# Kernel optimization log

Measured on AMD Instinct MI355X. Metric: run time of the kernel, lower is better.

The kernel has to match this reference:

```python
import jax, jax.numpy as jnp
import numpy as np
from jax import lax

B, S, D, T = 128, 512, 512, 64
OUT = 3


def setup_inputs() -> dict:
    key = jax.random.key(0)
    ks = jax.random.split(key, 16)
    sd = 0.05
    return {
        "e_all": jax.random.normal(ks[0], (B, S, D), jnp.float32),
        "e_last": jax.random.normal(ks[1], (1, B, D), jnp.float32),
        "target": jax.random.normal(ks[2], (B, T, OUT), jnp.float32),
        # attention params
        "Wa": jax.random.normal(ks[3], (D, D), jnp.float32) * sd,
        "ba": jnp.zeros((D,), jnp.float32),
        "Ua": jax.random.normal(ks[4], (D, D), jnp.float32) * sd,
        "bu": jnp.zeros((D,), jnp.float32),
        "Va_w": jax.random.normal(ks[5], (1, D), jnp.float32) * sd,
        "Va_b": jnp.zeros((1,), jnp.float32),
        # GRU params (PyTorch layout: [3D, in], gates order r,z,n)
        "W_ih": jax.random.normal(ks[6], (3 * D, D + OUT), jnp.float32) * sd,
        "b_ih": jnp.zeros((3 * D,), jnp.float32),
        "W_hh": jax.random.normal(ks[7], (3 * D, D), jnp.float32) * sd,
        "b_hh": jnp.zeros((3 * D,), jnp.float32),
        # output projection
        "W_out": jax.random.normal(ks[8], (OUT, D), jnp.float32) * sd,
        "b_out": jnp.zeros((OUT,), jnp.float32),
    }


def reference(e_all, e_last, target, Wa, ba, Ua, bu, Va_w, Va_b,
              W_ih, b_ih, W_hh, b_hh, W_out, b_out):
    # Precompute Ua(keys): keys are fixed across timesteps (same math as per-step).
    Uk = jnp.einsum('bsd,ed->bse', e_all, Ua) + bu        # [B,S,D]
    va = Va_w[0]                                          # [D]

    def step(h, x):
        # h: [B,D] decoder hidden; x: [B,3] decoder input (dropout is eval/identity)
        q = h @ Wa.T + ba                                  # [B,D]
        scores = jnp.einsum('bsd,d->bs', jnp.tanh(q[:, None, :] + Uk), va) + Va_b[0]
        w = jax.nn.softmax(scores, axis=-1)                # [B,S]
        ctx = jnp.einsum('bs,bsd->bd', w, e_all)           # [B,D]
        gin = jnp.concatenate([ctx, x], axis=-1)           # [B,D+3]  (attn first)
        gi = gin @ W_ih.T + b_ih                           # [B,3D]
        gh = h @ W_hh.T + b_hh                             # [B,3D]
        i_r, i_z, i_n = jnp.split(gi, 3, axis=-1)
        h_r, h_z, h_n = jnp.split(gh, 3, axis=-1)
        r = jax.nn.sigmoid(i_r + h_r)
        z = jax.nn.sigmoid(i_z + h_z)
        n = jnp.tanh(i_n + r * h_n)
        h_new = (1.0 - z) * n + z * h                      # [B,D]
        out = h_new @ W_out.T + b_out                      # [B,3]
        return h_new, (out, w)

    # teacher forcing: step 0 sees zeros, step i sees target[:, i-1]
    xs = jnp.concatenate([jnp.zeros((1, B, OUT), e_all.dtype),
                          jnp.swapaxes(target[:, :T - 1, :], 0, 1)], axis=0)  # [T,B,3]
    hT, (outs, attns) = lax.scan(step, e_last[0], xs)
    d_outputs = jnp.swapaxes(outs, 0, 1)     # [B,T,3]
    cross_attn = jnp.swapaxes(attns, 0, 1)   # [B,T,S]
    return d_outputs, hT[None], cross_attn
```

## Files before the change

### kernel.cpp

```cpp
#include <hip/hip_runtime.h>
#include <cstdint>

constexpr int BB = 128;
constexpr int SS = 512;
constexpr int DD = 512;
constexpr int TT = 64;
constexpr int OO = 3;

constexpr float C2LE = 2.8853900817779268f;

typedef __attribute__((ext_vector_type(8))) short bf16x8;
typedef __attribute__((ext_vector_type(4))) float f32x4;
typedef unsigned int u32x4 __attribute__((ext_vector_type(4)));

__device__ __forceinline__ float tanh_fast(float x) {
  float e = __expf(2.0f * x);
  return 1.0f - 2.0f / (e + 1.0f);
}
__device__ __forceinline__ float sigmoid_fast(float x) {
  return 1.0f / (1.0f + __expf(-x));
}
__device__ __forceinline__ unsigned short f2bf(float f) {
  uint32_t u = __float_as_uint(f);
  uint32_t r = (u + 0x7FFFu + ((u >> 16) & 1u)) >> 16;
  return (unsigned short)r;
}
__device__ __forceinline__ float bf2f(unsigned short h) {
  return __uint_as_float((uint32_t)h << 16);
}
__device__ __forceinline__ float2 bfx2(uint32_t u) {
  float2 r;
  r.x = __uint_as_float(u << 16);
  r.y = __uint_as_float(u & 0xFFFF0000u);
  return r;
}
__device__ __forceinline__ float fexp2(float x) {
#if __has_builtin(__builtin_amdgcn_exp2f)
  return __builtin_amdgcn_exp2f(x);
#else
  return exp2f(x);
#endif
}
__device__ __forceinline__ float frcp(float x) {
#if __has_builtin(__builtin_amdgcn_rcpf)
  return __builtin_amdgcn_rcpf(x);
#else
  return 1.0f / x;
#endif
}

__device__ __forceinline__ void gstore(float* p, float v) {
  __hip_atomic_store(p, v, __ATOMIC_RELAXED, __HIP_MEMORY_SCOPE_AGENT);
}
__device__ __forceinline__ float gload(const float* p) {
  return __hip_atomic_load(p, __ATOMIC_RELAXED, __HIP_MEMORY_SCOPE_AGENT);
}

__device__ __forceinline__ void pair_barrier(unsigned int* cnt,
                                             unsigned int target) {
  asm volatile("s_waitcnt vmcnt(0)" ::: "memory");
  __syncthreads();
  if (threadIdx.x == 0) {
    __hip_atomic_fetch_add(cnt, 1u, __ATOMIC_RELAXED, __HIP_MEMORY_SCOPE_AGENT);
    while (__hip_atomic_load(cnt, __ATOMIC_RELAXED,
                             __HIP_MEMORY_SCOPE_AGENT) < target)
      __builtin_amdgcn_s_sleep(2);
  }
  __syncthreads();
}

__global__ __launch_bounds__(256) void gemm_uk_mfma(
    const unsigned short* __restrict__ A, const unsigned short* __restrict__ Bw,
    const float* __restrict__ bias, unsigned short* __restrict__ Uk) {
  __shared__ unsigned short Asb[128 * 40];
  __shared__ unsigned short Bsb[128 * 40];
  const int tid = threadIdx.x;
  const int m0 = blockIdx.y * 128, n0 = blockIdx.x * 128;
  const int w = tid >> 6, l = tid & 63;
  const int wr = w >> 1, wc = w & 1;
  const int lm = l & 15, kg = l >> 4;

  f32x4 acc[4][4] = {};

  for (int kc = 0; kc < 512; kc += 32) {
    uint4 av[2], bv[2];
#pragma unroll
    for (int p = 0; p < 2; ++p) {
      int u = tid + p * 256;
      int r = u >> 2, ko = (u & 3) * 8;
      av[p] = *(const uint4*)(A + (size_t)(m0 + r) * 512 + kc + ko);
      bv[p] = *(const uint4*)(Bw + (size_t)(n0 + r) * 512 + kc + ko);
    }
    __syncthreads();
#pragma unroll
    for (int p = 0; p < 2; ++p) {
      int u = tid + p * 256;
      int r = u >> 2, ko = (u & 3) * 8;
      *(uint4*)&Asb[r * 40 + ko] = av[p];
      *(uint4*)&Bsb[r * 40 + ko] = bv[p];
    }
    __syncthreads();
    bf16x8 af[4], bfr[4];
#pragma unroll
    for (int i = 0; i < 4; ++i) {
      af[i]  = *(const bf16x8*)&Asb[(wr * 64 + i * 16 + lm) * 40 + kg * 8];
      bfr[i] = *(const bf16x8*)&Bsb[(wc * 64 + i * 16 + lm) * 40 + kg * 8];
    }
#pragma unroll
    for (int i = 0; i < 4; ++i)
#pragma unroll
      for (int j = 0; j < 4; ++j)
        acc[i][j] = __builtin_amdgcn_mfma_f32_16x16x32_bf16(af[i], bfr[j],
                                                            acc[i][j], 0, 0, 0);
  }

  const int row_base = m0 + wr * 64;
  const int col_base = n0 + wc * 64;
#pragma unroll
  for (int j = 0; j < 4; ++j) {
    const int col = col_base + j * 16 + lm;
    const float bu = bias[col];
#pragma unroll
    for (int i = 0; i < 4; ++i) {
      const int r0 = row_base + i * 16 + kg * 4;
#pragma unroll
      for (int rr = 0; rr < 4; ++rr)
        Uk[(size_t)(r0 + rr) * 512 + col] = f2bf(C2LE * (acc[i][j][rr] + bu));
    }
  }
}

__global__ __launch_bounds__(256) void conv_bf(const float* __restrict__ in,
                                               unsigned short* __restrict__ outp) {
  size_t idx = ((size_t)blockIdx.x * 256 + threadIdx.x) * 8;
  const float4* p = (const float4*)(in + idx);
  float4 a = p[0], b = p[1];
  uint4 r;
  r.x = f2bf(a.x) | ((uint32_t)f2bf(a.y) << 16);
  r.y = f2bf(a.z) | ((uint32_t)f2bf(a.w) << 16);
  r.z = f2bf(b.x) | ((uint32_t)f2bf(b.y) << 16);
  r.w = f2bf(b.z) | ((uint32_t)f2bf(b.w) << 16);
  *(uint4*)(outp + idx) = r;
}

__global__ void prep_wq2t(const float* __restrict__ Wa,
                          unsigned short* __restrict__ Wq2t) {
  int idx = blockIdx.x * 256 + threadIdx.x;
  int k = idx >> 9, j = idx & 511;
  Wq2t[idx] = f2bf(C2LE * Wa[(size_t)j * DD + k]);
}

__global__ void prep_wihT(const float* __restrict__ W_ih,
                          unsigned short* __restrict__ WihT) {
  int idx = blockIdx.x * 256 + threadIdx.x;
  int k = idx / 1536, col = idx % 1536;
  WihT[idx] = f2bf(W_ih[(size_t)col * (DD + OO) + k]);
}

__global__ void prep_whhT(const float* __restrict__ Whh,
                          unsigned short* __restrict__ WhhT) {
  int idx = blockIdx.x * 256 + threadIdx.x;
  int k = idx / 1536, col = idx % 1536;
  WhhT[idx] = f2bf(Whh[(size_t)col * DD + k]);
}

__global__ void prep_bq(const float* __restrict__ ba, float* __restrict__ bq) {
  int j = blockIdx.x * 256 + threadIdx.x;
  bq[j] = C2LE * ba[j];
}

__global__ __launch_bounds__(1024, 1) void decode_pairs(
    const unsigned short* __restrict__ Uk2, const unsigned short* __restrict__ e_bf,
    const unsigned short* __restrict__ Wq2t, const unsigned short* __restrict__ WihT,
    const unsigned short* __restrict__ WhhT, const float* __restrict__ bq,
    const float* __restrict__ W_ih, const float* __restrict__ b_ih,
    const float* __restrict__ b_hh, const float* __restrict__ e_last,
    const float* __restrict__ target, const float* __restrict__ Va_w,
    const float* __restrict__ W_out, const float* __restrict__ b_out,
    float* __restrict__ ctxp, char* __restrict__ bars,
    float* __restrict__ out_d, float* __restrict__ out_hT,
    float* __restrict__ out_attn) {
  const int blk = blockIdx.x, tid = threadIdx.x;
  const int b = blk >> 1, half = blk & 1;
  char* bar_base = bars + (size_t)b * 256;
  unsigned int* cnt = (unsigned int*)bar_base;
  float* stat4 = (float*)(bar_base + 16);
  unsigned int bc = 0;

  __shared__ float va_s[528];
  __shared__ float qv_s[528];
  __shared__ float h_s[512];
  __shared__ float pd_s[512];
  __shared__ float u_s[256];
  __shared__ float w_s[256];
  __shared__ float red_s[16];
  __shared__ float part[16 * 520];
  __shared__ float ctx_s[512];
  __shared__ float gis[768];
  __shared__ float ghs[768];

  float wxr0 = 0.f, wxr1 = 0.f, wxr2 = 0.f, bihr = 0.f, bhhr = 0.f;
  if (tid < 768) {
    const int gate = tid >> 8, dl = tid & 255;
    const int row = gate * 512 + half * 256 + dl;
    const float* wp = W_ih + (size_t)row * (DD + OO) + DD;
    wxr0 = wp[0]; wxr1 = wp[1]; wxr2 = wp[2];
    bihr = b_ih[row]; bhhr = b_hh[row];
  }
  if (tid < 512) va_s[(tid >> 7) * 132 + (tid & 127)] = Va_w[tid];
  __syncthreads();

  for (int t = 0; t < TT; ++t) {
    if (tid < 512) {
      h_s[tid] = (t == 0) ? e_last[(size_t)b * 512 + tid]
                          : gload(out_hT + (size_t)b * 512 + tid);
    }
    __syncthreads();
    {
      const int col = tid & 511, kb = tid >> 9;
      const unsigned short* wp = Wq2t + (size_t)(kb * 256) * 512 + col;
      const float* hb = &h_s[kb * 256];
      float acc = 0.f;
      for (int k0 = 0; k0 < 256; k0 += 8) {
        float4 hv0 = *(const float4*)&hb[k0];
        float4 hv1 = *(const float4*)&hb[k0 + 4];
        acc += hv0.x * bf2f(wp[(size_t)(k0 + 0) * 512]);
        acc += hv0.y * bf2f(wp[(size_t)(k0 + 1) * 512]);
        acc += hv0.z * bf2f(wp[(size_t)(k0 + 2) * 512]);
        acc += hv0.w * bf2f(wp[(size_t)(k0 + 3) * 512]);
        acc += hv1.x * bf2f(wp[(size_t)(k0 + 4) * 512]);
        acc += hv1.y * bf2f(wp[(size_t)(k0 + 5) * 512]);
        acc += hv1.z * bf2f(wp[(size_t)(k0 + 6) * 512]);
        acc += hv1.w * bf2f(wp[(size_t)(k0 + 7) * 512]);
      }
      if (kb) pd_s[col] = acc;
      __syncthreads();
      if (!kb) {
        float q = acc + pd_s[col] + bq[col];
        qv_s[(col >> 7) * 132 + (col & 127)] = q;
      }
      if (half == 0 && t > 0 && tid >= 512 && tid < 704) {
        const int o = (tid - 512) >> 6, ln = tid & 63;
        const float* wrow = W_out + (size_t)o * DD;
        float a = 0.f;
        for (int i = ln; i < DD; i += 64) a += h_s[i] * wrow[i];
#pragma unroll
        for (int off = 32; off; off >>= 1) a += __shfl_xor(a, off);
        if (ln == 0)
          out_d[((size_t)b * TT + (t - 1)) * OO + o] = a + b_out[o];
      }
    }
    __syncthreads();
    {
      const int sl = tid >> 2, qp = tid & 3;
      const u32x4* up = (const u32x4*)(Uk2 +
          ((size_t)b * SS + half * 256 + sl) * DD + qp * 128);
      const float* qb = &qv_s[qp * 132];
      const float* vb = &va_s[qp * 132];
      float acc = 0.f;
#pragma unroll 4
      for (int j = 0; j < 16; ++j) {
        u32x4 u = __builtin_nontemporal_load(up + j);
        float4 q0 = *(const float4*)&qb[j * 8], q1 = *(const float4*)&qb[j * 8 + 4];
        float4 v0 = *(const float4*)&vb[j * 8], v1 = *(const float4*)&vb[j * 8 + 4];
        float2 e0 = bfx2(u[0]), e1 = bfx2(u[1]), e2 = bfx2(u[2]), e3 = bfx2(u[3]);
        acc += v0.x * frcp(1.f + fexp2(q0.x + e0.x));
        acc += v0.y * frcp(1.f + fexp2(q0.y + e0.y));
        acc += v0.z * frcp(1.f + fexp2(q0.z + e1.x));
        acc += v0.w * frcp(1.f + fexp2(q0.w + e1.y));
        acc += v1.x * frcp(1.f + fexp2(q1.x + e2.x));
        acc += v1.y * frcp(1.f + fexp2(q1.y + e2.y));
        acc += v1.z * frcp(1.f + fexp2(q1.z + e3.x));
        acc += v1.w * frcp(1.f + fexp2(q1.w + e3.y));
      }
      acc += __shfl_xor(acc, 1);
      acc += __shfl_xor(acc, 2);
      if (qp == 0) u_s[sl] = -2.f * acc;
    }
    __syncthreads();
    {
      const int w4 = tid >> 6;
      float y = (tid < 256) ? u_s[tid] : -3.0e38f;
      float m = y;
#pragma unroll
      for (int off = 32; off; off >>= 1) m = fmaxf(m, __shfl_xor(m, off));
      if (w4 < 4 && (tid & 63) == 0) red_s[w4] = m;
      __syncthreads();
      const float gm =
          fmaxf(fmaxf(red_s[0], red_s[1]), fmaxf(red_s[2], red_s[3]));
      float e = (tid < 256) ? __expf(y - gm) : 0.f;
      float sm = e;
#pragma unroll
      for (int off = 32; off; off >>= 1) sm += __shfl_xor(sm, off);
      if (w4 < 4 && (tid & 63) == 0) red_s[8 + w4] = sm;
      __syncthreads();
      if (tid < 256) u_s[tid] = e;
      if (tid == 0) {
        gstore(&stat4[half * 2], gm);
        gstore(&stat4[half * 2 + 1],
               red_s[8] + red_s[9] + red_s[10] + red_s[11]);
      }
    }
    pair_barrier(cnt, 2 * (++bc));

    if (tid == 0) {
      red_s[8] = gload(&stat4[0]);
      red_s[9] = gload(&stat4[1]);
      red_s[10] = gload(&stat4[2]);
      red_s[11] = gload(&stat4[3]);
    }
    __syncthreads();
    {
      const float m0 = red_s[8], l0 = red_s[9], m1 = red_s[10], l1 = red_s[11];
      const float M = fmaxf(m0, m1);
      const float invZ = frcp(l0 * __expf(m0 - M) + l1 * __expf(m1 - M));
      const float al = __expf((half ? m1 : m0) - M) * invZ;
      if (tid < 256) {
        float wv = u_s[tid] * al;
        w_s[tid] = wv;
        __builtin_nontemporal_store(
            wv, out_attn + ((size_t)b * TT + t) * SS + half * 256 + tid);
      }
    }
    __syncthreads();
    {
      const int dsl = tid & 63, sg = tid >> 6;
      const unsigned short* eb =
          e_bf + ((size_t)b * SS + half * 256 + sg * 16) * DD + dsl * 8;
      float a0 = 0.f, a1 = 0.f, a2 = 0.f, a3 = 0.f;
      float a4 = 0.f, a5 = 0.f, a6 = 0.f, a7 = 0.f;
#pragma unroll 4
      for (int si = 0; si < 16; ++si) {
        u32x4 u = __builtin_nontemporal_load((const u32x4*)(eb + (size_t)si * DD));
        float ws = w_s[sg * 16 + si];
        float2 p0 = bfx2(u[0]), p1 = bfx2(u[1]), p2 = bfx2(u[2]), p3 = bfx2(u[3]);
        a0 += ws * p0.x; a1 += ws * p0.y;
        a2 += ws * p1.x; a3 += ws * p1.y;
        a4 += ws * p2.x; a5 += ws * p2.y;
        a6 += ws * p3.x; a7 += ws * p3.y;
      }
      float* pr = &part[sg * 520 + dsl * 8];
      float4 lo = {a0, a1, a2, a3}, hi = {a4, a5, a6, a7};
      *(float4*)&pr[0] = lo;
      *(float4*)&pr[4] = hi;
    }
    __syncthreads();
    if (tid < 512) {
      float r = 0.f;
#pragma unroll
      for (int sg = 0; sg < 16; ++sg) r += part[sg * 520 + tid];
      gstore(&ctxp[((size_t)b * 2 + half) * 512 + tid], r);
    }
    pair_barrier(cnt, 2 * (++bc));

    if (tid < 512)
      ctx_s[tid] = gload(&ctxp[(size_t)b * 2 * 512 + tid]) +
                   gload(&ctxp[((size_t)b * 2 + 1) * 512 + tid]);
    __syncthreads();
    if (tid < 768) {
      const int gate = tid >> 8, dl = tid & 255;
      const int col = gate * 512 + half * 256 + dl;
      const unsigned short* wi = WihT + col;
      const unsigned short* wh = WhhT + col;
      float ai = 0.f, ah = 0.f;
      for (int k0 = 0; k0 < 512; k0 += 8) {
        float4 c0 = *(const float4*)&ctx_s[k0];
        float4 c1 = *(const float4*)&ctx_s[k0 + 4];
        float4 h0 = *(const float4*)&h_s[k0];
        float4 h1 = *(const float4*)&h_s[k0 + 4];
        ai += c0.x * bf2f(wi[(size_t)(k0 + 0) * 1536]);
        ah += h0.x * bf2f(wh[(size_t)(k0 + 0) * 1536]);
        ai += c0.y * bf2f(wi[(size_t)(k0 + 1) * 1536]);
        ah += h0.y * bf2f(wh[(size_t)(k0 + 1) * 1536]);
        ai += c0.z * bf2f(wi[(size_t)(k0 + 2) * 1536]);
        ah += h0.z * bf2f(wh[(size_t)(k0 + 2) * 1536]);
        ai += c0.w * bf2f(wi[(size_t)(k0 + 3) * 1536]);
        ah += h0.w * bf2f(wh[(size_t)(k0 + 3) * 1536]);
        ai += c1.x * bf2f(wi[(size_t)(k0 + 4) * 1536]);
        ah += h1.x * bf2f(wh[(size_t)(k0 + 4) * 1536]);
        ai += c1.y * bf2f(wi[(size_t)(k0 + 5) * 1536]);
        ah += h1.y * bf2f(wh[(size_t)(k0 + 5) * 1536]);
        ai += c1.z * bf2f(wi[(size_t)(k0 + 6) * 1536]);
        ah += h1.z * bf2f(wh[(size_t)(k0 + 6) * 1536]);
        ai += c1.w * bf2f(wi[(size_t)(k0 + 7) * 1536]);
        ah += h1.w * bf2f(wh[(size_t)(k0 + 7) * 1536]);
      }
      float x0 = 0.f, x1 = 0.f, x2 = 0.f;
      if (t > 0) {
        const float* xp = target + ((size_t)b * TT + (t - 1)) * OO;
        x0 = xp[0]; x1 = xp[1]; x2 = xp[2];
      }
      gis[tid] = ai + bihr + x0 * wxr0 + x1 * wxr1 + x2 * wxr2;
      ghs[tid] = ah + bhhr;
    }
    __syncthreads();
    if (tid < 256) {
      const int d = half * 256 + tid;
      float r_ = sigmoid_fast(gis[tid] + ghs[tid]);
      float z_ = sigmoid_fast(gis[256 + tid] + ghs[256 + tid]);
      float n_ = tanh_fast(gis[512 + tid] + r_ * ghs[512 + tid]);
      float hnew = (1.f - z_) * n_ + z_ * h_s[d];
      gstore(out_hT + (size_t)b * 512 + d, hnew);
    }
    pair_barrier(cnt, 2 * (++bc));
  }

  if (half == 0) {
    if (tid < 512) h_s[tid] = gload(out_hT + (size_t)b * 512 + tid);
    __syncthreads();
    if (tid < 192) {
      const int o = tid >> 6, ln = tid & 63;
      const float* wrow = W_out + (size_t)o * DD;
      float a = 0.f;
      for (int i = ln; i < DD; i += 64) a += h_s[i] * wrow[i];
#pragma unroll
      for (int off = 32; off; off >>= 1) a += __shfl_xor(a, off);
      if (ln == 0)
        out_d[((size_t)b * TT + (TT - 1)) * OO + o] = a + b_out[o];
    }
  }
}

extern "C" void kernel_launch(void* const* d_in, const int* in_sizes, int n_in,
                              void* d_out, int out_size, void* d_ws, size_t ws_size,
                              hipStream_t stream) {
  const float* e_all  = (const float*)d_in[0];
  const float* e_last = (const float*)d_in[1];
  const float* target = (const float*)d_in[2];
  const float* Wa     = (const float*)d_in[3];
  const float* ba     = (const float*)d_in[4];
  const float* Ua     = (const float*)d_in[5];
  const float* bu     = (const float*)d_in[6];
  const float* Va_w   = (const float*)d_in[7];
  const float* W_ih   = (const float*)d_in[9];
  const float* b_ih   = (const float*)d_in[10];
  const float* W_hh   = (const float*)d_in[11];
  const float* b_hh   = (const float*)d_in[12];
  const float* W_out  = (const float*)d_in[13];
  const float* b_out  = (const float*)d_in[14];

  float* out      = (float*)d_out;
  float* out_d    = out;
  float* out_hT   = out + (size_t)BB * TT * OO;
  float* out_attn = out_hT + (size_t)BB * DD;

  char* wsB = (char*)d_ws;
  unsigned short* Uk2   = (unsigned short*)wsB;
  unsigned short* e_bfp = (unsigned short*)(wsB + 67108864);
  unsigned short* Wq2t  = (unsigned short*)(wsB + 134217728);
  unsigned short* WihT  = (unsigned short*)(wsB + 134742016);
  unsigned short* WhhT  = (unsigned short*)(wsB + 136314880);
  float* bq             = (float*)(wsB + 137887744);
  float* ctxp           = (float*)(wsB + 137889792);
  char* bars            = wsB + 138414080;
  unsigned short* Ua_bf = (unsigned short*)(wsB + 137889792);

  prep_wq2t<<<(DD * DD) / 256, 256, 0, stream>>>(Wa, Wq2t);
  prep_wihT<<<(512 * 1536) / 256, 256, 0, stream>>>(W_ih, WihT);
  prep_whhT<<<(512 * 1536) / 256, 256, 0, stream>>>(W_hh, WhhT);
  prep_bq<<<2, 256, 0, stream>>>(ba, bq);
  conv_bf<<<(BB * SS * DD) / (8 * 256), 256, 0, stream>>>(e_all, e_bfp);
  conv_bf<<<(DD * DD) / (8 * 256), 256, 0, stream>>>(Ua, Ua_bf);
  gemm_uk_mfma<<<dim3(DD / 128, (BB * SS) / 128), 256, 0, stream>>>(
      e_bfp, Ua_bf, bu, Uk2);

  hipMemsetAsync(bars, 0, 128 * 256, stream);

  decode_pairs<<<2 * BB, 1024, 0, stream>>>(
      Uk2, e_bfp, Wq2t, WihT, WhhT, bq, W_ih, b_ih, b_hh, e_last, target,
      Va_w, W_out, b_out, ctxp, bars, out_d, out_hT, out_attn);
}
```

Before: 5.523 ms.

## Split decode across quads of blocks by hidden dim, two batches per group

Reorganizes the persistent decoder so each group of four blocks handles two batch rows, with each block owning a 128-wide slice of the hidden dimension rather than half the sequence. Uk is stored in a transposed [b][dq][d][s] layout so each block streams only its own slice, and every weight read in the GRU and query GEMVs is reused across two batch rows. The output projection is folded into the step as per-slice partial sums. In exchange, each step now needs three cross-block barriers over four blocks, with score and context partials exchanged through global memory, and the per-element Uk and e loads are narrower scalar bf16 loads.

```diff
diff --git a/kernel.cpp b/kernel.cpp
--- a/kernel.cpp
+++ b/kernel.cpp
@@ -11,7 +11,6 @@
 
 typedef __attribute__((ext_vector_type(8))) short bf16x8;
 typedef __attribute__((ext_vector_type(4))) float f32x4;
-typedef unsigned int u32x4 __attribute__((ext_vector_type(4)));
 
 __device__ __forceinline__ float tanh_fast(float x) {
   float e = __expf(2.0f * x);
@@ -27,12 +26,6 @@
 }
 __device__ __forceinline__ float bf2f(unsigned short h) {
   return __uint_as_float((uint32_t)h << 16);
-}
-__device__ __forceinline__ float2 bfx2(uint32_t u) {
-  float2 r;
-  r.x = __uint_as_float(u << 16);
-  r.y = __uint_as_float(u & 0xFFFF0000u);
-  return r;
 }
 __device__ __forceinline__ float fexp2(float x) {
 #if __has_builtin(__builtin_amdgcn_exp2f)
@@ -56,8 +49,8 @@
   return __hip_atomic_load(p, __ATOMIC_RELAXED, __HIP_MEMORY_SCOPE_AGENT);
 }
 
-__device__ __forceinline__ void pair_barrier(unsigned int* cnt,
-                                             unsigned int target) {
+__device__ __forceinline__ void grp_barrier(unsigned int* cnt,
+                                            unsigned int target) {
   asm volatile("s_waitcnt vmcnt(0)" ::: "memory");
   __syncthreads();
   if (threadIdx.x == 0) {
@@ -71,7 +64,7 @@
 
 __global__ __launch_bounds__(256) void gemm_uk_mfma(
     const unsigned short* __restrict__ A, const unsigned short* __restrict__ Bw,
-    const float* __restrict__ bias, unsigned short* __restrict__ Uk) {
+    const float* __restrict__ bias, unsigned short* __restrict__ Ukq) {
   __shared__ unsigned short Asb[128 * 40];
   __shared__ unsigned short Bsb[128 * 40];
   const int tid = threadIdx.x;
@@ -119,13 +112,18 @@
 #pragma unroll
   for (int j = 0; j < 4; ++j) {
     const int col = col_base + j * 16 + lm;
-    const float bu = bias[col];
+    const int dqi = col >> 7, dpi = col & 127;
+    const float buv = bias[col];
 #pragma unroll
     for (int i = 0; i < 4; ++i) {
       const int r0 = row_base + i * 16 + kg * 4;
-#pragma unroll
-      for (int rr = 0; rr < 4; ++rr)
-        Uk[(size_t)(r0 + rr) * 512 + col] = f2bf(C2LE * (acc[i][j][rr] + bu));
+      const int bb = r0 >> 9, ss = r0 & 511;
+      ushort4 pk;
+      pk.x = f2bf(C2LE * (acc[i][j][0] + buv));
+      pk.y = f2bf(C2LE * (acc[i][j][1] + buv));
+      pk.z = f2bf(C2LE * (acc[i][j][2] + buv));
+      pk.w = f2bf(C2LE * (acc[i][j][3] + buv));
+      *(ushort4*)&Ukq[(((size_t)bb * 4 + dqi) * 128 + dpi) * 512 + ss] = pk;
     }
   }
 }
@@ -169,255 +167,215 @@
   bq[j] = C2LE * ba[j];
 }
 
-__global__ __launch_bounds__(1024, 1) void decode_pairs(
-    const unsigned short* __restrict__ Uk2, const unsigned short* __restrict__ e_bf,
+__global__ __launch_bounds__(1024, 1) void decode_quads(
+    const unsigned short* __restrict__ Ukq, const unsigned short* __restrict__ e_bf,
     const unsigned short* __restrict__ Wq2t, const unsigned short* __restrict__ WihT,
     const unsigned short* __restrict__ WhhT, const float* __restrict__ bq,
     const float* __restrict__ W_ih, const float* __restrict__ b_ih,
     const float* __restrict__ b_hh, const float* __restrict__ e_last,
     const float* __restrict__ target, const float* __restrict__ Va_w,
     const float* __restrict__ W_out, const float* __restrict__ b_out,
-    float* __restrict__ ctxp, char* __restrict__ bars,
+    float* __restrict__ scoresP, float* __restrict__ ctxg,
+    float* __restrict__ op, char* __restrict__ bars,
     float* __restrict__ out_d, float* __restrict__ out_hT,
     float* __restrict__ out_attn) {
   const int blk = blockIdx.x, tid = threadIdx.x;
-  const int b = blk >> 1, half = blk & 1;
-  char* bar_base = bars + (size_t)b * 256;
-  unsigned int* cnt = (unsigned int*)bar_base;
-  float* stat4 = (float*)(bar_base + 16);
+  const int g = blk >> 2, dq = blk & 3;
+  const int b0 = g * 2;
+  unsigned int* cnt = (unsigned int*)(bars + (size_t)g * 256);
   unsigned int bc = 0;
 
-  __shared__ float va_s[528];
-  __shared__ float qv_s[528];
-  __shared__ float h_s[512];
-  __shared__ float pd_s[512];
-  __shared__ float u_s[256];
-  __shared__ float w_s[256];
-  __shared__ float red_s[16];
-  __shared__ float part[16 * 520];
-  __shared__ float ctx_s[512];
-  __shared__ float gis[768];
-  __shared__ float ghs[768];
-
-  float wxr0 = 0.f, wxr1 = 0.f, wxr2 = 0.f, bihr = 0.f, bhhr = 0.f;
-  if (tid < 768) {
-    const int gate = tid >> 8, dl = tid & 255;
-    const int row = gate * 512 + half * 256 + dl;
+  __shared__ float h_s[2][512];
+  __shared__ float q2_sl[2][128];
+  __shared__ float pdq[3][2][128];
+  __shared__ float va_sl[128];
+  __shared__ float w_s[2][512];
+  __shared__ float red_s[2][16];
+  __shared__ float ctp[3][2][128];
+  __shared__ float c_s[2][512];
+  __shared__ f32x4 pd4[384];
+  __shared__ float gi_s[2][384];
+  __shared__ float gh_s[2][384];
+  __shared__ float hn_s[2][128];
+  __shared__ float x_s[2][3];
+
+  if (tid < 128) va_sl[tid] = Va_w[dq * 128 + tid];
+  float wx0 = 0.f, wx1 = 0.f, wx2 = 0.f, bi_r = 0.f, bh_r = 0.f;
+  if (tid < 384) {
+    const int cc = tid & 127, gate = (tid >> 7) % 3;
+    const int row = gate * 512 + dq * 128 + cc;
     const float* wp = W_ih + (size_t)row * (DD + OO) + DD;
-    wxr0 = wp[0]; wxr1 = wp[1]; wxr2 = wp[2];
-    bihr = b_ih[row]; bhhr = b_hh[row];
-  }
-  if (tid < 512) va_s[(tid >> 7) * 132 + (tid & 127)] = Va_w[tid];
+    wx0 = wp[0]; wx1 = wp[1]; wx2 = wp[2];
+    bi_r = b_ih[row]; bh_r = b_hh[row];
+  }
   __syncthreads();
 
   for (int t = 0; t < TT; ++t) {
-    if (tid < 512) {
-      h_s[tid] = (t == 0) ? e_last[(size_t)b * 512 + tid]
-                          : gload(out_hT + (size_t)b * 512 + tid);
-    }
-    __syncthreads();
-    {
-      const int col = tid & 511, kb = tid >> 9;
-      const unsigned short* wp = Wq2t + (size_t)(kb * 256) * 512 + col;
-      const float* hb = &h_s[kb * 256];
+    {
+      const int bl = tid >> 9, d = tid & 511;
+      h_s[bl][d] = (t == 0) ? e_last[(size_t)(b0 + bl) * 512 + d]
+                            : gload(out_hT + (size_t)(b0 + bl) * 512 + d);
+    }
+    if (dq == 0 && t > 0 && tid >= 1018) {
+      const int u = tid - 1018, bl = u / 3, o = u % 3;
+      float s = 0.f;
+#pragma unroll
+      for (int q = 0; q < 4; ++q)
+        s += gload(&op[(((size_t)(b0 + bl)) * 4 + q) * 3 + o]);
+      out_d[((size_t)(b0 + bl) * TT + (t - 1)) * OO + o] = s + b_out[o];
+    }
+    __syncthreads();
+    {
+      const int col = tid & 127, bl = (tid >> 7) & 1, kb = tid >> 8;
+      const int colg = dq * 128 + col;
       float acc = 0.f;
-      for (int k0 = 0; k0 < 256; k0 += 8) {
-        float4 hv0 = *(const float4*)&hb[k0];
-        float4 hv1 = *(const float4*)&hb[k0 + 4];
-        acc += hv0.x * bf2f(wp[(size_t)(k0 + 0) * 512]);
-        acc += hv0.y * bf2f(wp[(size_t)(k0 + 1) * 512]);
-        acc += hv0.z * bf2f(wp[(size_t)(k0 + 2) * 512]);
-        acc += hv0.w * bf2f(wp[(size_t)(k0 + 3) * 512]);
-        acc += hv1.x * bf2f(wp[(size_t)(k0 + 4) * 512]);
-        acc += hv1.y * bf2f(wp[(size_t)(k0 + 5) * 512]);
-        acc += hv1.z * bf2f(wp[(size_t)(k0 + 6) * 512]);
-        acc += hv1.w * bf2f(wp[(size_t)(k0 + 7) * 512]);
+#pragma unroll 8
+      for (int k = kb * 128; k < kb * 128 + 128; ++k)
+        acc += h_s[bl][k] * bf2f(Wq2t[(size_t)k * 512 + colg]);
+      if (kb) pdq[kb - 1][bl][col] = acc;
+      __syncthreads();
+      if (kb == 0)
+        q2_sl[bl][col] = acc + pdq[0][bl][col] + pdq[1][bl][col] +
+                         pdq[2][bl][col] + bq[colg];
+    }
+    __syncthreads();
+    {
+      const int bl = tid >> 9, s = tid & 511;
+      const unsigned short* up =
+          Ukq + (((size_t)(b0 + bl) * 4 + dq) * 128) * 512 + s;
+      float acc = 0.f;
+#pragma unroll 8
+      for (int dpi = 0; dpi < 128; ++dpi) {
+        unsigned short uv = __builtin_nontemporal_load(up + (size_t)dpi * 512);
+        acc += va_sl[dpi] * frcp(1.f + fexp2(q2_sl[bl][dpi] + bf2f(uv)));
       }
-      if (kb) pd_s[col] = acc;
+      gstore(&scoresP[(((size_t)(b0 + bl)) * 4 + dq) * 512 + s], acc);
+    }
+    grp_barrier(cnt, 4 * (++bc));
+
+    {
+      const int bl = tid >> 9, s = tid & 511;
+      const float* sp = &scoresP[((size_t)(b0 + bl)) * 4 * 512 + s];
+      float y = -2.f * (gload(sp) + gload(sp + 512) + gload(sp + 1024) +
+                        gload(sp + 1536));
+      float m = y;
+#pragma unroll
+      for (int off = 32; off; off >>= 1) m = fmaxf(m, __shfl_xor(m, off));
+      const int wv = (tid >> 6) & 7;
+      if ((tid & 63) == 0) red_s[bl][wv] = m;
       __syncthreads();
-      if (!kb) {
-        float q = acc + pd_s[col] + bq[col];
-        qv_s[(col >> 7) * 132 + (col & 127)] = q;
+      float gm = red_s[bl][0];
+#pragma unroll
+      for (int i = 1; i < 8; ++i) gm = fmaxf(gm, red_s[bl][i]);
+      float e = __expf(y - gm);
+      float sm = e;
+#pragma unroll
+      for (int off = 32; off; off >>= 1) sm += __shfl_xor(sm, off);
+      if ((tid & 63) == 0) red_s[bl][8 + wv] = sm;
+      __syncthreads();
+      float Z = red_s[bl][8];
+#pragma unroll
+      for (int i = 1; i < 8; ++i) Z += red_s[bl][8 + i];
+      float wgt = e * frcp(Z);
+      w_s[bl][s] = wgt;
+      if (s >= dq * 128 && s < dq * 128 + 128)
+        __builtin_nontemporal_store(
+            wgt, out_attn + ((size_t)(b0 + bl) * TT + t) * SS + s);
+    }
+    __syncthreads();
+    {
+      const int ch = tid >> 8, bl = (tid >> 7) & 1, dpi = tid & 127;
+      const unsigned short* eb =
+          e_bf + ((size_t)(b0 + bl) * 512 + ch * 128) * 512 + dq * 128 + dpi;
+      float acc = 0.f;
+#pragma unroll 8
+      for (int si = 0; si < 128; ++si) {
+        unsigned short uv = __builtin_nontemporal_load(eb + (size_t)si * 512);
+        acc += w_s[bl][ch * 128 + si] * bf2f(uv);
       }
-      if (half == 0 && t > 0 && tid >= 512 && tid < 704) {
-        const int o = (tid - 512) >> 6, ln = tid & 63;
-        const float* wrow = W_out + (size_t)o * DD;
-        float a = 0.f;
-        for (int i = ln; i < DD; i += 64) a += h_s[i] * wrow[i];
-#pragma unroll
-        for (int off = 32; off; off >>= 1) a += __shfl_xor(a, off);
-        if (ln == 0)
-          out_d[((size_t)b * TT + (t - 1)) * OO + o] = a + b_out[o];
+      if (ch) ctp[ch - 1][bl][dpi] = acc;
+      __syncthreads();
+      if (ch == 0)
+        gstore(&ctxg[(size_t)(b0 + bl) * 512 + dq * 128 + dpi],
+               acc + ctp[0][bl][dpi] + ctp[1][bl][dpi] + ctp[2][bl][dpi]);
+    }
+    grp_barrier(cnt, 4 * (++bc));
+
+    {
+      const int bl = tid >> 9, d = tid & 511;
+      c_s[bl][d] = gload(&ctxg[(size_t)(b0 + bl) * 512 + d]);
+    }
+    if (tid >= 1016 && tid < 1022) {
+      const int u = tid - 1016, bl = u / 3, o = u % 3;
+      x_s[bl][o] =
+          (t > 0) ? target[((size_t)(b0 + bl) * TT + (t - 1)) * OO + o] : 0.f;
+    }
+    __syncthreads();
+    {
+      float ai0 = 0.f, ai1 = 0.f, ah0 = 0.f, ah1 = 0.f;
+      int cc = 0, gate = 0;
+      if (tid < 768) {
+        cc = tid & 127; gate = (tid >> 7) % 3;
+        const int kb = tid / 384;
+        const int colg = gate * 512 + dq * 128 + cc;
+        const unsigned short* wi = WihT + colg;
+        const unsigned short* wh = WhhT + colg;
+#pragma unroll 8
+        for (int k = kb * 256; k < kb * 256 + 256; ++k) {
+          float wiv = bf2f(wi[(size_t)k * 1536]);
+          float whv = bf2f(wh[(size_t)k * 1536]);
+          ai0 += c_s[0][k] * wiv; ai1 += c_s[1][k] * wiv;
+          ah0 += h_s[0][k] * whv; ah1 += h_s[1][k] * whv;
+        }
+        if (tid >= 384) {
+          f32x4 v = {ai0, ai1, ah0, ah1};
+          pd4[gate * 128 + cc] = v;
+        }
       }
-    }
-    __syncthreads();
-    {
-      const int sl = tid >> 2, qp = tid & 3;
-      const u32x4* up = (const u32x4*)(Uk2 +
-          ((size_t)b * SS + half * 256 + sl) * DD + qp * 128);
-      const float* qb = &qv_s[qp * 132];
-      const float* vb = &va_s[qp * 132];
-      float acc = 0.f;
-#pragma unroll 4
-      for (int j = 0; j < 16; ++j) {
-        u32x4 u = __builtin_nontemporal_load(up + j);
-        float4 q0 = *(const float4*)&qb[j * 8], q1 = *(const float4*)&qb[j * 8 + 4];
-        float4 v0 = *(const float4*)&vb[j * 8], v1 = *(const float4*)&vb[j * 8 + 4];
-        float2 e0 = bfx2(u[0]), e1 = bfx2(u[1]), e2 = bfx2(u[2]), e3 = bfx2(u[3]);
-        acc += v0.x * frcp(1.f + fexp2(q0.x + e0.x));
-        acc += v0.y * frcp(1.f + fexp2(q0.y + e0.y));
-        acc += v0.z * frcp(1.f + fexp2(q0.z + e1.x));
-        acc += v0.w * frcp(1.f + fexp2(q0.w + e1.y));
-        acc += v1.x * frcp(1.f + fexp2(q1.x + e2.x));
-        acc += v1.y * frcp(1.f + fexp2(q1.y + e2.y));
-        acc += v1.z * frcp(1.f + fexp2(q1.z + e3.x));
-        acc += v1.w * frcp(1.f + fexp2(q1.w + e3.y));
+      __syncthreads();
+      if (tid < 384) {
+        f32x4 p = pd4[gate * 128 + cc];
+        const int gc = gate * 128 + cc;
+        gi_s[0][gc] = ai0 + p[0] + bi_r + x_s[0][0] * wx0 + x_s[0][1] * wx1 +
+                      x_s[0][2] * wx2;
+        gi_s[1][gc] = ai1 + p[1] + bi_r + x_s[1][0] * wx0 + x_s[1][1] * wx1 +
+                      x_s[1][2] * wx2;
+        gh_s[0][gc] = ah0 + p[2] + bh_r;
+        gh_s[1][gc] = ah1 + p[3] + bh_r;
       }
-      acc += __shfl_xor(acc, 1);
-      acc += __shfl_xor(acc, 2);
-      if (qp == 0) u_s[sl] = -2.f * acc;
-    }
-    __syncthreads();
-    {
-      const int w4 = tid >> 6;
-      float y = (tid < 256) ? u_s[tid] : -3.0e38f;
-      float m = y;
-#pragma unroll
-      for (int off = 32; off; off >>= 1) m = fmaxf(m, __shfl_xor(m, off));
-      if (w4 < 4 && (tid & 63) == 0) red_s[w4] = m;
-      __syncthreads();
-      const float gm =
-          fmaxf(fmaxf(red_s[0], red_s[1]), fmaxf(red_s[2], red_s[3]));
-      float e = (tid < 256) ? __expf(y - gm) : 0.f;
-      float sm = e;
-#pragma unroll
-      for (int off = 32; off; off >>= 1) sm += __shfl_xor(sm, off);
-      if (w4 < 4 && (tid & 63) == 0) red_s[8 + w4] = sm;
-      __syncthreads();
-      if (tid < 256) u_s[tid] = e;
-      if (tid == 0) {
-        gstore(&stat4[half * 2], gm);
-        gstore(&stat4[half * 2 + 1],
-               red_s[8] + red_s[9] + red_s[10] + red_s[11]);
-      }
-    }
-    pair_barrier(cnt, 2 * (++bc));
-
-    if (tid == 0) {
-      red_s[8] = gload(&stat4[0]);
-      red_s[9] = gload(&stat4[1]);
-      red_s[10] = gload(&stat4[2]);
-      red_s[11] = gload(&stat4[3]);
-    }
-    __syncthreads();
-    {
-      const float m0 = red_s[8], l0 = red_s[9], m1 = red_s[10], l1 = red_s[11];
-      const float M = fmaxf(m0, m1);
-      const float invZ = frcp(l0 * __expf(m0 - M) + l1 * __expf(m1 - M));
-      const float al = __expf((half ? m1 : m0) - M) * invZ;
-      if (tid < 256) {
-        float wv = u_s[tid] * al;
-        w_s[tid] = wv;
-        __builtin_nontemporal_store(
-            wv, out_attn + ((size_t)b * TT + t) * SS + half * 256 + tid);
-      }
-    }
-    __syncthreads();
-    {
-      const int dsl = tid & 63, sg = tid >> 6;
-      const unsigned short* eb =
-          e_bf + ((size_t)b * SS + half * 256 + sg * 16) * DD + dsl * 8;
-      float a0 = 0.f, a1 = 0.f, a2 = 0.f, a3 = 0.f;
-      float a4 = 0.f, a5 = 0.f, a6 = 0.f, a7 = 0.f;
-#pragma unroll 4
-      for (int si = 0; si < 16; ++si) {
-        u32x4 u = __builtin_nontemporal_load((const u32x4*)(eb + (size_t)si * DD));
-        float ws = w_s[sg * 16 + si];
-        float2 p0 = bfx2(u[0]), p1 = bfx2(u[1]), p2 = bfx2(u[2]), p3 = bfx2(u[3]);
-        a0 += ws * p0.x; a1 += ws * p0.y;
-        a2 += ws * p1.x; a3 += ws * p1.y;
-        a4 += ws * p2.x; a5 += ws * p2.y;
-        a6 += ws * p3.x; a7 += ws * p3.y;
-      }
-      float* pr = &part[sg * 520 + dsl * 8];
-      float4 lo = {a0, a1, a2, a3}, hi = {a4, a5, a6, a7};
-      *(float4*)&pr[0] = lo;
-      *(float4*)&pr[4] = hi;
-    }
-    __syncthreads();
-    if (tid < 512) {
-      float r = 0.f;
-#pragma unroll
-      for (int sg = 0; sg < 16; ++sg) r += part[sg * 520 + tid];
-      gstore(&ctxp[((size_t)b * 2 + half) * 512 + tid], r);
-    }
-    pair_barrier(cnt, 2 * (++bc));
-
-    if (tid < 512)
-      ctx_s[tid] = gload(&ctxp[(size_t)b * 2 * 512 + tid]) +
-                   gload(&ctxp[((size_t)b * 2 + 1) * 512 + tid]);
-    __syncthreads();
-    if (tid < 768) {
-      const int gate = tid >> 8, dl = tid & 255;
-      const int col = gate * 512 + half * 256 + dl;
-      const unsigned short* wi = WihT + col;
-      const unsigned short* wh = WhhT + col;
-      float ai = 0.f, ah = 0.f;
-      for (int k0 = 0; k0 < 512; k0 += 8) {
-        float4 c0 = *(const float4*)&ctx_s[k0];
-        float4 c1 = *(const float4*)&ctx_s[k0 + 4];
-        float4 h0 = *(const float4*)&h_s[k0];
-        float4 h1 = *(const float4*)&h_s[k0 + 4];
-        ai += c0.x * bf2f(wi[(size_t)(k0 + 0) * 1536]);
-        ah += h0.x * bf2f(wh[(size_t)(k0 + 0) * 1536]);
-        ai += c0.y * bf2f(wi[(size_t)(k0 + 1) * 1536]);
-        ah += h0.y * bf2f(wh[(size_t)(k0 + 1) * 1536]);
-        ai += c0.z * bf2f(wi[(size_t)(k0 + 2) * 1536]);
-        ah += h0.z * bf2f(wh[(size_t)(k0 + 2) * 1536]);
-        ai += c0.w * bf2f(wi[(size_t)(k0 + 3) * 1536]);
-        ah += h0.w * bf2f(wh[(size_t)(k0 + 3) * 1536]);
-        ai += c1.x * bf2f(wi[(size_t)(k0 + 4) * 1536]);
-        ah += h1.x * bf2f(wh[(size_t)(k0 + 4) * 1536]);
-        ai += c1.y * bf2f(wi[(size_t)(k0 + 5) * 1536]);
-        ah += h1.y * bf2f(wh[(size_t)(k0 + 5) * 1536]);
-        ai += c1.z * bf2f(wi[(size_t)(k0 + 6) * 1536]);
-        ah += h1.z * bf2f(wh[(size_t)(k0 + 6) * 1536]);
-        ai += c1.w * bf2f(wi[(size_t)(k0 + 7) * 1536]);
-        ah += h1.w * bf2f(wh[(size_t)(k0 + 7) * 1536]);
-      }
-      float x0 = 0.f, x1 = 0.f, x2 = 0.f;
-      if (t > 0) {
-        const float* xp = target + ((size_t)b * TT + (t - 1)) * OO;
-        x0 = xp[0]; x1 = xp[1]; x2 = xp[2];
-      }
-      gis[tid] = ai + bihr + x0 * wxr0 + x1 * wxr1 + x2 * wxr2;
-      ghs[tid] = ah + bhhr;
     }
     __syncthreads();
     if (tid < 256) {
-      const int d = half * 256 + tid;
-      float r_ = sigmoid_fast(gis[tid] + ghs[tid]);
-      float z_ = sigmoid_fast(gis[256 + tid] + ghs[256 + tid]);
-      float n_ = tanh_fast(gis[512 + tid] + r_ * ghs[512 + tid]);
-      float hnew = (1.f - z_) * n_ + z_ * h_s[d];
-      gstore(out_hT + (size_t)b * 512 + d, hnew);
-    }
-    pair_barrier(cnt, 2 * (++bc));
-  }
-
-  if (half == 0) {
-    if (tid < 512) h_s[tid] = gload(out_hT + (size_t)b * 512 + tid);
-    __syncthreads();
-    if (tid < 192) {
-      const int o = tid >> 6, ln = tid & 63;
-      const float* wrow = W_out + (size_t)o * DD;
-      float a = 0.f;
-      for (int i = ln; i < DD; i += 64) a += h_s[i] * wrow[i];
-#pragma unroll
-      for (int off = 32; off; off >>= 1) a += __shfl_xor(a, off);
+      const int bl = tid >> 7, cc = tid & 127;
+      const int d = dq * 128 + cc;
+      float r_ = sigmoid_fast(gi_s[bl][cc] + gh_s[bl][cc]);
+      float z_ = sigmoid_fast(gi_s[bl][128 + cc] + gh_s[bl][128 + cc]);
+      float n_ = tanh_fast(gi_s[bl][256 + cc] + r_ * gh_s[bl][256 + cc]);
+      float hnew = (1.f - z_) * n_ + z_ * h_s[bl][d];
+      gstore(out_hT + (size_t)(b0 + bl) * 512 + d, hnew);
+      hn_s[bl][cc] = hnew;
+    }
+    __syncthreads();
+    if (tid >= 256 && tid < 640) {
+      const int u = tid - 256, grp = u >> 6, ln = u & 63;
+      const int o = grp % 3, bl = grp / 3;
+      const float* wrow = W_out + (size_t)o * DD + dq * 128;
+      float acc = hn_s[bl][ln] * wrow[ln] + hn_s[bl][ln + 64] * wrow[ln + 64];
+#pragma unroll
+      for (int off = 32; off; off >>= 1) acc += __shfl_xor(acc, off);
       if (ln == 0)
-        out_d[((size_t)b * TT + (TT - 1)) * OO + o] = a + b_out[o];
-    }
+        gstore(&op[(((size_t)(b0 + bl)) * 4 + dq) * 3 + o], acc);
+    }
+    grp_barrier(cnt, 4 * (++bc));
+  }
+
+  if (dq == 0 && tid >= 1018) {
+    const int u = tid - 1018, bl = u / 3, o = u % 3;
+    float s = 0.f;
+#pragma unroll
+    for (int q = 0; q < 4; ++q)
+      s += gload(&op[(((size_t)(b0 + bl)) * 4 + q) * 3 + o]);
+    out_d[((size_t)(b0 + bl) * TT + (TT - 1)) * OO + o] = s + b_out[o];
   }
 }
 
@@ -445,14 +403,16 @@
   float* out_attn = out_hT + (size_t)BB * DD;
 
   char* wsB = (char*)d_ws;
-  unsigned short* Uk2   = (unsigned short*)wsB;
+  unsigned short* Ukq   = (unsigned short*)wsB;
   unsigned short* e_bfp = (unsigned short*)(wsB + 67108864);
   unsigned short* Wq2t  = (unsigned short*)(wsB + 134217728);
   unsigned short* WihT  = (unsigned short*)(wsB + 134742016);
   unsigned short* WhhT  = (unsigned short*)(wsB + 136314880);
   float* bq             = (float*)(wsB + 137887744);
-  float* ctxp           = (float*)(wsB + 137889792);
-  char* bars            = wsB + 138414080;
+  float* scoresP        = (float*)(wsB + 137889792);
+  float* ctxg           = (float*)(wsB + 138938368);
+  float* op             = (float*)(wsB + 139200512);
+  char* bars            = wsB + 139206656;
   unsigned short* Ua_bf = (unsigned short*)(wsB + 137889792);
 
   prep_wq2t<<<(DD * DD) / 256, 256, 0, stream>>>(Wa, Wq2t);
@@ -462,11 +422,11 @@
   conv_bf<<<(BB * SS * DD) / (8 * 256), 256, 0, stream>>>(e_all, e_bfp);
   conv_bf<<<(DD * DD) / (8 * 256), 256, 0, stream>>>(Ua, Ua_bf);
   gemm_uk_mfma<<<dim3(DD / 128, (BB * SS) / 128), 256, 0, stream>>>(
-      e_bfp, Ua_bf, bu, Uk2);
-
-  hipMemsetAsync(bars, 0, 128 * 256, stream);
-
-  decode_pairs<<<2 * BB, 1024, 0, stream>>>(
-      Uk2, e_bfp, Wq2t, WihT, WhhT, bq, W_ih, b_ih, b_hh, e_last, target,
-      Va_w, W_out, b_out, ctxp, bars, out_d, out_hT, out_attn);
-}
+      e_bfp, Ua_bf, bu, Ukq);
+
+  hipMemsetAsync(bars, 0, 64 * 256, stream);
+
+  decode_quads<<<256, 1024, 0, stream>>>(
+      Ukq, e_bfp, Wq2t, WihT, WhhT, bq, W_ih, b_ih, b_hh, e_last, target,
+      Va_w, W_out, b_out, scoresP, ctxg, op, bars, out_d, out_hT, out_attn);
+}
```

Result: faster. 4.678 ms (-15.3%).
